# Optimization experiments

Measured on AMD Instinct MI355X. Metric: run time of the kernel, lower is better.

The kernel has to match this reference:

```python
import jax, jax.numpy as jnp
import numpy as np

B, S, D = 2, 2048, 2048
H, DK, DV, L = 16, 128, 128, 64


def setup_inputs() -> dict:
    key = jax.random.key(0)
    ks = jax.random.split(key, 12)
    s = lambda k, shape, fan_in: jax.random.normal(k, shape, jnp.float32) / np.sqrt(fan_in)
    return {
        "queries": jax.random.normal(ks[0], (B, S, D), jnp.float32),
        "keys": jax.random.normal(ks[1], (B, S, D), jnp.float32),
        "values": jax.random.normal(ks[2], (B, S, D), jnp.float32),
        "Wq": s(ks[3], (D, H * DK), D), "bq": jnp.zeros((H * DK,), jnp.float32),
        "Wlk": s(ks[4], (D, H * L), D), "blk": jnp.zeros((H * L,), jnp.float32),
        "Wlv": s(ks[5], (D, H * L), D), "blv": jnp.zeros((H * L,), jnp.float32),
        "Wkr": s(ks[6], (L, DK), L),
        "Wvr": s(ks[7], (L, DV), L),
        "Wout": s(ks[8], (H * DV, D), H * DV), "bout": jnp.zeros((D,), jnp.float32),
    }


def reference(queries, keys, values, Wq, bq, Wlk, blk, Wlv, blv, Wkr, Wvr, Wout, bout):
    b, sq, _ = queries.shape
    sk = keys.shape[1]
    # projections -> [b, h, s, d]
    q = (queries @ Wq + bq).reshape(b, sq, H, DK).transpose(0, 2, 1, 3)
    lk = (keys @ Wlk + blk).reshape(b, sk, H, L).transpose(0, 2, 1, 3)
    lv = (values @ Wlv + blv).reshape(b, sk, H, L).transpose(0, 2, 1, 3)
    k = lk @ Wkr  # [b,h,sk,DK] latent -> key reconstruction
    v = lv @ Wvr  # [b,h,sk,DV]
    scores = jnp.einsum('bhqd,bhkd->bhqk', q, k) / np.sqrt(DK).astype(np.float32)
    causal = jnp.triu(jnp.ones((sq, sk), dtype=bool), k=1)
    scores = jnp.where(causal, -jnp.inf, scores)
    attn = jax.nn.softmax(scores, axis=-1)
    out = jnp.einsum('bhqk,bhkd->bhqd', attn, v)
    out = out.transpose(0, 2, 1, 3).reshape(b, sq, H * DV)
    return out @ Wout + bout
```

## Files before the change

kernel.cpp:

```cpp
#include <hip/hip_runtime.h>
#include <cstdint>
#include <cstddef>

typedef _Float16 f16;
typedef __attribute__((ext_vector_type(8))) _Float16 f16x8;
typedef __attribute__((ext_vector_type(4))) _Float16 f16x4;
typedef __attribute__((ext_vector_type(4))) float f32x4;

constexpr int kB  = 2;
constexpr int kS  = 2048;
constexpr int kD  = 2048;
constexpr int kH  = 16;
constexpr int kL  = 64;
constexpr int kHL = kH * kL;
constexpr int kBS = kB * kS;

__device__ __forceinline__ void load_lds16(const void* g, void* l) {
  __builtin_amdgcn_global_load_lds((const __attribute__((address_space(1))) void*)g,
                                   (__attribute__((address_space(3))) void*)l, 16, 0, 0);
}

__device__ __forceinline__ f32x4 mfma16(f16x8 a, f16x8 b, f32x4 c) {
  return __builtin_amdgcn_mfma_f32_16x16x32_f16(a, b, c, 0, 0, 0);
}

__global__ void cast4(const float* __restrict__ a, const float* __restrict__ b,
                      const float* __restrict__ c, const float* __restrict__ d,
                      f16* __restrict__ oa, f16* __restrict__ ob,
                      f16* __restrict__ oc, f16* __restrict__ od) {
  const int z = blockIdx.z;
  int i = blockIdx.x * 256 + threadIdx.x;
  if (z == 3 && i >= kD * kD / 4) return;
  const float* in = z == 0 ? a : z == 1 ? b : z == 2 ? c : d;
  f16* out = z == 0 ? oa : z == 1 ? ob : z == 2 ? oc : od;
  float4 f = ((const float4*)in)[i];
  f16x4 o; o[0] = (f16)f.x; o[1] = (f16)f.y; o[2] = (f16)f.z; o[3] = (f16)f.w;
  ((f16x4*)out)[i] = o;
}

__device__ __forceinline__ void transpose_body(const float* __restrict__ in,
                                               f16* __restrict__ out, int R, int C) {
  const int r0 = blockIdx.y * 64, c0 = blockIdx.x * 64;
  __shared__ float tile[64][65];
  const int t = threadIdx.x;
  const int cc = t & 63, rr = t >> 6;
#pragma unroll
  for (int p = 0; p < 16; p++) {
    int r = p * 4 + rr;
    tile[r][cc] = in[(size_t)(r0 + r) * C + c0 + cc];
  }
  __syncthreads();
#pragma unroll
  for (int p = 0; p < 16; p++) {
    int c = p * 4 + rr;
    out[(size_t)(c0 + c) * R + r0 + cc] = (f16)tile[cc][c];
  }
}

__global__ __launch_bounds__(256) void transpose3(const float* __restrict__ Wlk,
                                                  const float* __restrict__ Wlv,
                                                  const float* __restrict__ Wout,
                                                  f16* __restrict__ Wlkt,
                                                  f16* __restrict__ Wlvt,
                                                  f16* __restrict__ WoutT) {
  const int z = blockIdx.z;
  if (z < 2 && blockIdx.x >= 16) return;
  if (z == 0) transpose_body(Wlk, Wlkt, 2048, 1024);
  else if (z == 1) transpose_body(Wlv, Wlvt, 2048, 1024);
  else transpose_body(Wout, WoutT, 2048, 2048);
}

__global__ void fold_bq(const float* __restrict__ bq, const float* __restrict__ Wkr,
                        float* __restrict__ bql) {
  int hl = blockIdx.x * 256 + threadIdx.x;
  if (hl >= kHL) return;
  int h = hl >> 6, l = hl & 63;
  float s = 0.f;
  for (int c = 0; c < 128; c++) s += bq[h * 128 + c] * Wkr[l * 128 + c];
  bql[hl] = s;
}

__global__ __launch_bounds__(256) void fold2(const float* __restrict__ Wkr,
                                             const float* __restrict__ Wvr,
                                             const f16* __restrict__ Wq16,
                                             const f16* __restrict__ WoutT,
                                             f16* __restrict__ Wqlt,
                                             f16* __restrict__ W2t) {
  __shared__ f16 sA[64 * 136];
  __shared__ f16 sB[128 * 128];
  const int z = blockIdx.z;
  const int h = blockIdx.y;
  const int d0 = blockIdx.x * 128;
  const float* Wsm = z ? Wvr : Wkr;
  const f16* Bsrc = (z ? WoutT : Wq16) + h * 128;
  const int tid = threadIdx.x;
  const int w = tid >> 6, lane = tid & 63;
  const int quad = lane >> 4, l16 = lane & 15;

#pragma unroll
  for (int it = 0; it < 8; it++) {
    int i = it * 256 + tid;
    float4 f = ((const float4*)Wsm)[i];
    int e = i * 4, r = e >> 7, c = e & 127;
    f16x4 o; o[0] = (f16)f.x; o[1] = (f16)f.y; o[2] = (f16)f.z; o[3] = (f16)f.w;
    *(f16x4*)&sA[r * 136 + c] = o;
  }
#pragma unroll
  for (int c = 0; c < 8; c++) {
    int rbase = w * 32 + c * 4;
    load_lds16(Bsrc + (size_t)(d0 + rbase + (lane >> 4)) * 2048 + (lane & 15) * 8,
               &sB[rbase * 128]);
  }
  __syncthreads();

  if (z == 0) {
    f32x4 acc[4][2];
    for (int mt = 0; mt < 4; mt++)
      for (int nt = 0; nt < 2; nt++) acc[mt][nt] = (f32x4){0.f, 0.f, 0.f, 0.f};
#pragma unroll
    for (int ks = 0; ks < 4; ks++) {
      f16x8 af[4], bf[2];
#pragma unroll
      for (int mt = 0; mt < 4; mt++)
        af[mt] = *(const f16x8*)&sA[(mt * 16 + l16) * 136 + ks * 32 + quad * 8];
#pragma unroll
      for (int nt = 0; nt < 2; nt++)
        bf[nt] = *(const f16x8*)&sB[(w * 32 + nt * 16 + l16) * 128 + ks * 32 + quad * 8];
#pragma unroll
      for (int mt = 0; mt < 4; mt++)
#pragma unroll
        for (int nt = 0; nt < 2; nt++) acc[mt][nt] = mfma16(af[mt], bf[nt], acc[mt][nt]);
    }
#pragma unroll
    for (int mt = 0; mt < 4; mt++)
#pragma unroll
      for (int nt = 0; nt < 2; nt++)
#pragma unroll
        for (int r = 0; r < 4; r++) {
          int row = mt * 16 + quad * 4 + r;
          int col = d0 + w * 32 + nt * 16 + l16;
          Wqlt[(size_t)(h * 64 + row) * 2048 + col] = (f16)acc[mt][nt][r];
        }
  } else {
    f32x4 acc[2][4];
    for (int mt = 0; mt < 2; mt++)
      for (int nt = 0; nt < 4; nt++) acc[mt][nt] = (f32x4){0.f, 0.f, 0.f, 0.f};
#pragma unroll
    for (int ks = 0; ks < 4; ks++) {
      f16x8 af[2], bf[4];
#pragma unroll
      for (int mt = 0; mt < 2; mt++)
        af[mt] = *(const f16x8*)&sB[(w * 32 + mt * 16 + l16) * 128 + ks * 32 + quad * 8];
#pragma unroll
      for (int nt = 0; nt < 4; nt++)
        bf[nt] = *(const f16x8*)&sA[(nt * 16 + l16) * 136 + ks * 32 + quad * 8];
#pragma unroll
      for (int mt = 0; mt < 2; mt++)
#pragma unroll
        for (int nt = 0; nt < 4; nt++) acc[mt][nt] = mfma16(af[mt], bf[nt], acc[mt][nt]);
    }
#pragma unroll
    for (int mt = 0; mt < 2; mt++)
#pragma unroll
      for (int nt = 0; nt < 4; nt++)
#pragma unroll
        for (int r = 0; r < 4; r++) {
          int row = d0 + w * 32 + mt * 16 + quad * 4 + r;
          int col = nt * 16 + l16;
          W2t[(size_t)row * 1024 + h * 64 + col] = (f16)acc[mt][nt][r];
        }
  }
}

template <typename OutT, bool HAS_BIAS>
__device__ __forceinline__ void gemm_body(const f16* __restrict__ A, const f16* __restrict__ Bt,
                                          const float* __restrict__ bias, OutT* __restrict__ C,
                                          int N, int K, int m0, int n0) {
  __shared__ f16 sA[2][128 * 32];
  __shared__ f16 sB[2][128 * 32];
  const int tid = threadIdx.x;
  const int w = tid >> 6, lane = tid & 63;
  const int quad = lane >> 4, l16 = lane & 15;
  const int wm = w >> 1, wn = w & 1;

  const int srow = lane >> 2;
  const int schunk = (lane & 3) ^ ((lane >> 3) & 3);
  const f16* aptr = A + (size_t)(m0 + w * 32 + srow) * K + schunk * 8;
  const f16* bptr = Bt + (size_t)(n0 + w * 32 + srow) * K + schunk * 8;
  const int g0 = w * 1024;
  const int g1 = g0 + 512;

  const int xoff = (quad ^ ((l16 >> 1) & 3)) * 8;

  f32x4 acc[4][4];
  for (int i = 0; i < 4; i++)
    for (int j = 0; j < 4; j++) acc[i][j] = (f32x4){0.f, 0.f, 0.f, 0.f};

  load_lds16(aptr, &sA[0][g0]);
  load_lds16(aptr + (size_t)16 * K, &sA[0][g1]);
  load_lds16(bptr, &sB[0][g0]);
  load_lds16(bptr + (size_t)16 * K, &sB[0][g1]);
  int cur = 0;

  for (int k0 = 0; k0 < K; k0 += 32) {
    __syncthreads();
    if (k0 + 32 < K) {
      const f16* ap = aptr + k0 + 32;
      const f16* bp = bptr + k0 + 32;
      f16* dA = &sA[cur ^ 1][0];
      f16* dB = &sB[cur ^ 1][0];
      load_lds16(ap, dA + g0);
      load_lds16(ap + (size_t)16 * K, dA + g1);
      load_lds16(bp, dB + g0);
      load_lds16(bp + (size_t)16 * K, dB + g1);
    }
    const f16* sAc = &sA[cur][0];
    const f16* sBc = &sB[cur][0];
    f16x8 af[4], bfr[4];
#pragma unroll
    for (int mt = 0; mt < 4; mt++)
      af[mt] = *(const f16x8*)&sAc[(wm * 64 + mt * 16 + l16) * 32 + xoff];
#pragma unroll
    for (int nt = 0; nt < 4; nt++)
      bfr[nt] = *(const f16x8*)&sBc[(wn * 64 + nt * 16 + l16) * 32 + xoff];
#pragma unroll
    for (int mt = 0; mt < 4; mt++) {
#pragma unroll
      for (int nt = 0; nt < 4; nt++)
        acc[mt][nt] = mfma16(af[mt], bfr[nt], acc[mt][nt]);
    }
    cur ^= 1;
  }
#pragma unroll
  for (int mt = 0; mt < 4; mt++) {
#pragma unroll
    for (int nt = 0; nt < 4; nt++) {
      int col = n0 + wn * 64 + nt * 16 + l16;
      float bv = HAS_BIAS ? bias[col] : 0.f;
#pragma unroll
      for (int r = 0; r < 4; r++) {
        int row = m0 + wm * 64 + mt * 16 + quad * 4 + r;
        C[(size_t)row * N + col] = (OutT)(acc[mt][nt][r] + bv);
      }
    }
  }
}

__device__ __forceinline__ int xcd_swizzle(int flat, int nwg) {
  const int cpx = nwg >> 3;
  return (flat & 7) * cpx + (flat >> 3);
}

__global__ __launch_bounds__(256) void gemm3_f16(
    const f16* __restrict__ A0, const f16* __restrict__ A1, const f16* __restrict__ A2,
    const f16* __restrict__ B0, const f16* __restrict__ B1, const f16* __restrict__ B2,
    const float* __restrict__ c0, const float* __restrict__ c1, const float* __restrict__ c2,
    f16* __restrict__ C0, f16* __restrict__ C1, f16* __restrict__ C2, int N, int K) {
  const f16* A = blockIdx.z == 0 ? A0 : blockIdx.z == 1 ? A1 : A2;
  const f16* Bt = blockIdx.z == 0 ? B0 : blockIdx.z == 1 ? B1 : B2;
  const float* bias = blockIdx.z == 0 ? c0 : blockIdx.z == 1 ? c1 : c2;
  f16* C = blockIdx.z == 0 ? C0 : blockIdx.z == 1 ? C1 : C2;
  const int nx = gridDim.x;
  int swz = xcd_swizzle(blockIdx.y * nx + blockIdx.x, nx * gridDim.y);
  gemm_body<f16, true>(A, Bt, bias, C, N, K, (swz / nx) * 128, (swz % nx) * 128);
}

__global__ __launch_bounds__(256) void gemm_f32(const f16* __restrict__ A,
                                                const f16* __restrict__ Bt,
                                                const float* __restrict__ bias,
                                                float* __restrict__ C, int N, int K) {
  const int nx = gridDim.x;
  int swz = xcd_swizzle(blockIdx.y * nx + blockIdx.x, nx * gridDim.y);
  gemm_body<float, true>(A, Bt, bias, C, N, K, (swz / nx) * 128, (swz % nx) * 128);
}

__global__ __launch_bounds__(256) void transpose_lv(const f16* __restrict__ LV,
                                                    f16* __restrict__ LVt) {
  const int bh = blockIdx.y, b = bh >> 4, h = bh & 15;
  const int s0 = blockIdx.x * 64;
  __shared__ f16 tile[64][65];
  const int t = threadIdx.x;
  const int c0 = t & 63, r0 = t >> 6;
#pragma unroll
  for (int r = 0; r < 16; r++) {
    int s = r * 4 + r0;
    tile[s][c0] = LV[(size_t)(b * kS + s0 + s) * kHL + h * kL + c0];
  }
  __syncthreads();
#pragma unroll
  for (int r = 0; r < 16; r++) {
    int vl = r * 4 + r0;
    LVt[((size_t)bh * kL + vl) * kS + s0 + c0] = tile[c0][vl];
  }
}

__global__ __launch_bounds__(256) void attn(const f16* __restrict__ Qlat,
                                            const f16* __restrict__ LK,
                                            const f16* __restrict__ LVt,
                                            f16* __restrict__ Ctx) {
  const int bh = blockIdx.y, b = bh >> 4, h = bh & 15;
  const int pair = blockIdx.x;
  const int tid = threadIdx.x;
  const int w = tid >> 6, lane = tid & 63;
  const int quad = lane >> 4, l16 = lane & 15;

  __shared__ f16 sK[2][64 * 64];
  __shared__ f16 sV[2][64 * 64];
  __shared__ f16 sP[4][16 * 72];

  const f16* qbase = Qlat + (size_t)b * kS * kHL + h * kL;
  const f16* kbase = LK + (size_t)b * kS * kHL + h * kL;
  const f16* vbase = LVt + (size_t)bh * kL * kS;

  const float cscale = 0.08838834764831845f * 1.4426950408889634f;
  const int rowA = lane >> 3;
  const int colSw = (((lane & 7) ^ (lane >> 3)) << 3);
  const int sw0 = ((quad ^ (l16 & 7)) << 3);
  const int sw1 = (((4 + quad) ^ (l16 & 7)) << 3);

  for (int which = 0; which < 2; which++) {
    const int t = which ? (31 - pair) : pair;
    const int q0 = t * 64;
    const int qrow = q0 + w * 16 + l16;
    const int qg = qrow;
    const int ntile = t + 1;

    f16x8 aq[2];
#pragma unroll
    for (int ks = 0; ks < 2; ks++)
      aq[ks] = *(const f16x8*)(qbase + (size_t)qrow * kHL + ks * 32 + quad * 8);

    f32x4 acc[4];
    for (int nt = 0; nt < 4; nt++) acc[nt] = (f32x4){0.f, 0.f, 0.f, 0.f};
    float m_s = -3.0e38f;
    float l_part = 0.f;

    __syncthreads();
    {
      const int rl = w * 16;
      load_lds16(kbase + (size_t)(rl + rowA) * kHL + colSw, &sK[0][rl * 64]);
      load_lds16(vbase + (size_t)(rl + rowA) * kS + colSw, &sV[0][rl * 64]);
      load_lds16(kbase + (size_t)(rl + 8 + rowA) * kHL + colSw, &sK[0][(rl + 8) * 64]);
      load_lds16(vbase + (size_t)(rl + 8 + rowA) * kS + colSw, &sV[0][(rl + 8) * 64]);
    }
    int cur = 0;

    for (int it = 0; it < ntile; ++it) {
      const int kv0 = it * 64;
      __syncthreads();

      if (it + 1 < ntile) {
        const int nkv = kv0 + 64;
        f16* dK = &sK[cur ^ 1][0];
        f16* dV = &sV[cur ^ 1][0];
        const int rl = w * 16;
        load_lds16(kbase + (size_t)(nkv + rl + rowA) * kHL + colSw, dK + rl * 64);
        load_lds16(vbase + (size_t)(rl + rowA) * kS + nkv + colSw, dV + rl * 64);
        load_lds16(kbase + (size_t)(nkv + rl + 8 + rowA) * kHL + colSw, dK + (rl + 8) * 64);
        load_lds16(vbase + (size_t)(rl + 8 + rowA) * kS + nkv + colSw, dV + (rl + 8) * 64);
      }
      const f16* sKc = &sK[cur][0];
      const f16* sVc = &sV[cur][0];

      f32x4 sc[4];
      for (int nt = 0; nt < 4; nt++) sc[nt] = (f32x4){0.f, 0.f, 0.f, 0.f};
#pragma unroll
      for (int ks = 0; ks < 2; ks++) {
        const int sw = ks ? sw1 : sw0;
        f16x8 bk[4];
#pragma unroll
        for (int nt = 0; nt < 4; nt++)
          bk[nt] = *(const f16x8*)&sKc[(nt * 16 + l16) * 64 + sw];
#pragma unroll
        for (int nt = 0; nt < 4; nt++) sc[nt] = mfma16(bk[nt], aq[ks], sc[nt]);
      }

      if (kv0 == q0) {
#pragma unroll
        for (int nt = 0; nt < 4; nt++) {
#pragma unroll
          for (int r = 0; r < 4; r++) {
            int kvg = kv0 + nt * 16 + quad * 4 + r;
            if (kvg > qg) sc[nt][r] = -1.0e30f;
          }
        }
      }

      float tm = -3.0e38f;
#pragma unroll
      for (int nt = 0; nt < 4; nt++)
        tm = fmaxf(tm, fmaxf(fmaxf(sc[nt][0], sc[nt][1]), fmaxf(sc[nt][2], sc[nt][3])));
      tm = fmaxf(tm, __shfl_xor(tm, 16));
      tm = fmaxf(tm, __shfl_xor(tm, 32));
      const float tms = tm * cscale;

      if (!__all(tms <= m_s)) {
        const float mnew = fmaxf(m_s, tms);
        const float alpha = __builtin_amdgcn_exp2f(m_s - mnew);
        m_s = mnew;
        l_part *= alpha;
        float ar[4];
#pragma unroll
        for (int r = 0; r < 4; r++) ar[r] = __shfl(alpha, quad * 4 + r);
#pragma unroll
        for (int nt = 0; nt < 4; nt++)
#pragma unroll
          for (int r = 0; r < 4; r++) acc[nt][r] *= ar[r];
      }

      float ps = 0.f;
#pragma unroll
      for (int nt = 0; nt < 4; nt++) {
        f16x4 pk;
#pragma unroll
        for (int r = 0; r < 4; r++) {
          float p = __builtin_amdgcn_exp2f(__builtin_fmaf(sc[nt][r], cscale, -m_s));
          ps += p;
          pk[r] = (f16)p;
        }
        *(f16x4*)&sP[w][l16 * 72 + nt * 16 + quad * 4] = pk;
      }
      l_part += ps;

#pragma unroll
      for (int ks = 0; ks < 2; ks++) {
        const int sw = ks ? sw1 : sw0;
        f16x8 ap = *(const f16x8*)&sP[w][l16 * 72 + ks * 32 + quad * 8];
        f16x8 bv[4];
#pragma unroll
        for (int nt = 0; nt < 4; nt++)
          bv[nt] = *(const f16x8*)&sVc[(nt * 16 + l16) * 64 + sw];
#pragma unroll
        for (int nt = 0; nt < 4; nt++) acc[nt] = mfma16(ap, bv[nt], acc[nt]);
      }
      cur ^= 1;
    }

    float lfull = l_part;
    lfull += __shfl_xor(lfull, 16);
    lfull += __shfl_xor(lfull, 32);
    float inv[4];
#pragma unroll
    for (int r = 0; r < 4; r++) inv[r] = 1.f / __shfl(lfull, quad * 4 + r);
#pragma unroll
    for (int r = 0; r < 4; r++) {
      int qout = q0 + w * 16 + quad * 4 + r;
      size_t base = (size_t)(b * kS + qout) * kHL + h * kL;
#pragma unroll
      for (int nt = 0; nt < 4; nt++)
        Ctx[base + nt * 16 + l16] = (f16)(acc[nt][r] * inv[r]);
    }
  }
}

extern "C" void kernel_launch(void* const* d_in, const int* in_sizes, int n_in,
                              void* d_out, int out_size, void* d_ws, size_t ws_size,
                              hipStream_t stream) {
  (void)in_sizes; (void)n_in; (void)out_size; (void)ws_size;
  const float* queries = (const float*)d_in[0];
  const float* keys    = (const float*)d_in[1];
  const float* values  = (const float*)d_in[2];
  const float* Wq      = (const float*)d_in[3];
  const float* bq      = (const float*)d_in[4];
  const float* Wlk     = (const float*)d_in[5];
  const float* blk     = (const float*)d_in[6];
  const float* Wlv     = (const float*)d_in[7];
  const float* blv     = (const float*)d_in[8];
  const float* Wkr     = (const float*)d_in[9];
  const float* Wvr     = (const float*)d_in[10];
  const float* Wout    = (const float*)d_in[11];
  const float* bout    = (const float*)d_in[12];

  char* ws = (char*)d_ws;
  size_t off = 0;
  auto alloc = [&](size_t bytes) {
    void* p = ws + off;
    off += (bytes + 255) & ~(size_t)255;
    return p;
  };
  f16* qb    = (f16*)alloc((size_t)kBS * kD * 2);
  f16* kb    = (f16*)alloc((size_t)kBS * kD * 2);
  f16* vb    = (f16*)alloc((size_t)kBS * kD * 2);
  f16* Wqlt  = (f16*)alloc((size_t)kHL * kD * 2);
  f16* Wlkt  = (f16*)alloc((size_t)kHL * kD * 2);
  f16* Wlvt  = (f16*)alloc((size_t)kHL * kD * 2);
  f16* W2t   = (f16*)alloc((size_t)kD * kHL * 2);
  float* bql = (float*)alloc(kHL * 4);
  f16* Qlat  = (f16*)alloc((size_t)kBS * kHL * 2);
  f16* LKb   = (f16*)alloc((size_t)kBS * kHL * 2);
  f16* LVb   = (f16*)alloc((size_t)kBS * kHL * 2);
  f16* Wq16  = Qlat;
  f16* WoutT = LKb;
  f16* LVtb = qb;
  f16* Ctx  = kb;

  const int n4 = kBS * kD / 4;
  cast4<<<dim3(n4 / 256, 1, 4), 256, 0, stream>>>(queries, keys, values, Wq, qb, kb, vb, Wq16);
  transpose3<<<dim3(32, 32, 3), 256, 0, stream>>>(Wlk, Wlv, Wout, Wlkt, Wlvt, WoutT);
  fold_bq<<<kHL / 256, 256, 0, stream>>>(bq, Wkr, bql);
  fold2<<<dim3(16, 16, 2), 256, 0, stream>>>(Wkr, Wvr, Wq16, WoutT, Wqlt, W2t);

  gemm3_f16<<<dim3(kHL / 128, kBS / 128, 3), 256, 0, stream>>>(
      qb, kb, vb, Wqlt, Wlkt, Wlvt, bql, blk, blv, Qlat, LKb, LVb, kHL, kD);

  transpose_lv<<<dim3(kS / 64, kB * kH), 256, 0, stream>>>(LVb, LVtb);
  attn<<<dim3(16, kB * kH), 256, 0, stream>>>(Qlat, LKb, LVtb, Ctx);
  gemm_f32<<<dim3(kD / 128, kBS / 128), 256, 0, stream>>>(Ctx, W2t, bout, (float*)d_out, kD, kHL);
}
```

Baseline: 360.9 us.

## Triple-buffer GEMM LDS staging with explicit vmcnt waits and barriers

Replaces the double-buffered LDS pipeline in the shared GEMM body with a three-stage ring. Global-to-LDS loads are issued two tiles ahead, and the loop waits with explicit s_waitcnt vmcnt counts, so only the oldest tile must have landed before each barrier. This lets loads overlap more MFMA work and drops the barrier at the top of each iteration. In exchange it uses 50% more LDS, which may lower occupancy, and hand-written waitcnt values are fragile if the compiler reorders memory operations.

New measurement: 357.2 us. About the same (-1.0%).

```diff
diff --git a/kernel.cpp b/kernel.cpp
--- a/kernel.cpp
+++ b/kernel.cpp
@@ -176,8 +176,8 @@
 __device__ __forceinline__ void gemm_body(const f16* __restrict__ A, const f16* __restrict__ Bt,
                                           const float* __restrict__ bias, OutT* __restrict__ C,
                                           int N, int K, int m0, int n0) {
-  __shared__ f16 sA[2][128 * 32];
-  __shared__ f16 sB[2][128 * 32];
+  __shared__ f16 sAall[3 * 128 * 32];
+  __shared__ f16 sBall[3 * 128 * 32];
   const int tid = threadIdx.x;
   const int w = tid >> 6, lane = tid & 63;
   const int quad = lane >> 4, l16 = lane & 15;
@@ -196,51 +196,64 @@
   for (int i = 0; i < 4; i++)
     for (int j = 0; j < 4; j++) acc[i][j] = (f32x4){0.f, 0.f, 0.f, 0.f};
 
-  load_lds16(aptr, &sA[0][g0]);
-  load_lds16(aptr + (size_t)16 * K, &sA[0][g1]);
-  load_lds16(bptr, &sB[0][g0]);
-  load_lds16(bptr + (size_t)16 * K, &sB[0][g1]);
-  int cur = 0;
-
-  for (int k0 = 0; k0 < K; k0 += 32) {
-    __syncthreads();
-    if (k0 + 32 < K) {
-      const f16* ap = aptr + k0 + 32;
-      const f16* bp = bptr + k0 + 32;
-      f16* dA = &sA[cur ^ 1][0];
-      f16* dB = &sB[cur ^ 1][0];
-      load_lds16(ap, dA + g0);
-      load_lds16(ap + (size_t)16 * K, dA + g1);
-      load_lds16(bp, dB + g0);
-      load_lds16(bp + (size_t)16 * K, dB + g1);
-    }
-    const f16* sAc = &sA[cur][0];
-    const f16* sBc = &sB[cur][0];
+  auto stage = [&](int buf, int k0) {
+    f16* dA = &sAall[buf * 4096];
+    f16* dB = &sBall[buf * 4096];
+    load_lds16(aptr + k0, dA + g0);
+    load_lds16(aptr + (size_t)16 * K + k0, dA + g1);
+    load_lds16(bptr + k0, dB + g0);
+    load_lds16(bptr + (size_t)16 * K + k0, dB + g1);
+  };
+
+  const int nt = K >> 5;
+  stage(0, 0);
+  stage(1, 32);
+  asm volatile("s_waitcnt vmcnt(4)" ::: "memory");
+  __builtin_amdgcn_sched_barrier(0);
+  __builtin_amdgcn_s_barrier();
+  __builtin_amdgcn_sched_barrier(0);
+
+  int bc = 0, bs = 2;
+  for (int t = 0; t < nt; ++t) {
+    if (t + 2 < nt) stage(bs, (t + 2) * 32);
+    const f16* sAc = &sAall[bc * 4096];
+    const f16* sBc = &sBall[bc * 4096];
     f16x8 af[4], bfr[4];
 #pragma unroll
     for (int mt = 0; mt < 4; mt++)
       af[mt] = *(const f16x8*)&sAc[(wm * 64 + mt * 16 + l16) * 32 + xoff];
 #pragma unroll
-    for (int nt = 0; nt < 4; nt++)
-      bfr[nt] = *(const f16x8*)&sBc[(wn * 64 + nt * 16 + l16) * 32 + xoff];
+    for (int nf = 0; nf < 4; nf++)
+      bfr[nf] = *(const f16x8*)&sBc[(wn * 64 + nf * 16 + l16) * 32 + xoff];
 #pragma unroll
     for (int mt = 0; mt < 4; mt++) {
 #pragma unroll
-      for (int nt = 0; nt < 4; nt++)
-        acc[mt][nt] = mfma16(af[mt], bfr[nt], acc[mt][nt]);
-    }
-    cur ^= 1;
-  }
+      for (int nf = 0; nf < 4; nf++)
+        acc[mt][nf] = mfma16(af[mt], bfr[nf], acc[mt][nf]);
+    }
+    if (t + 1 < nt) {
+      if (t + 2 < nt)
+        asm volatile("s_waitcnt vmcnt(4)" ::: "memory");
+      else
+        asm volatile("s_waitcnt vmcnt(0)" ::: "memory");
+      __builtin_amdgcn_sched_barrier(0);
+      __builtin_amdgcn_s_barrier();
+      __builtin_amdgcn_sched_barrier(0);
+    }
+    bc = bc == 2 ? 0 : bc + 1;
+    bs = bs == 2 ? 0 : bs + 1;
+  }
+
 #pragma unroll
   for (int mt = 0; mt < 4; mt++) {
 #pragma unroll
-    for (int nt = 0; nt < 4; nt++) {
-      int col = n0 + wn * 64 + nt * 16 + l16;
+    for (int nf = 0; nf < 4; nf++) {
+      int col = n0 + wn * 64 + nf * 16 + l16;
       float bv = HAS_BIAS ? bias[col] : 0.f;
 #pragma unroll
       for (int r = 0; r < 4; r++) {
         int row = m0 + wm * 64 + mt * 16 + quad * 4 + r;
-        C[(size_t)row * N + col] = (OutT)(acc[mt][nt][r] + bv);
+        C[(size_t)row * N + col] = (OutT)(acc[mt][nf][r] + bv);
       }
     }
   }
```
